# Kernel tuning notes

Hardware: AMD Instinct MI355X
Metric: run time of the kernel (lower is better)

Reference implementation:

```python
import jax, jax.numpy as jnp
import numpy as np

B, C, L = 64, 64, 8192
EPS = float(np.finfo(np.float32).eps)  # matches np.finfo(np.float32).eps in the torch code


def setup_inputs() -> dict:
    key = jax.random.key(0)
    k1, k2, k3 = jax.random.split(key, 3)
    data = jax.random.normal(k1, (B, C, L), dtype=jnp.float32)
    idxes = jax.random.randint(k2, (B, L), 0, L).astype(jnp.int32)
    # prefix lengths in [1, L] so every slice is non-empty (ragged branch)
    zero_pos = jax.random.randint(k3, (B,), 1, L + 1)
    return {"data": data, "idxes": idxes, "zero_pos": zero_pos}


def reference(data, idxes, zero_pos):
    # data: [B, C, L]; per-batch mean/std over the prefix data[b, :, :zero_pos[b]]
    Bn, Cn, Ln = data.shape
    mask = (jnp.arange(Ln)[None, :] < zero_pos[:, None])[:, None, :].astype(data.dtype)  # [B,1,L]
    cnt = Cn * zero_pos.astype(data.dtype)  # [B] number of elements in each prefix
    mean = jnp.sum(data * mask, axis=(1, 2)) / cnt  # [B]
    diff = (data - mean[:, None, None]) * mask  # [B,C,L]
    var = jnp.sum(diff * diff, axis=(1, 2)) / (cnt - 1.0)  # unbiased, as torch.std
    std = jnp.sqrt(var)  # [B]
    out = (data - mean[:, None, None]) / (std[:, None, None] + EPS)
    return (out, idxes, zero_pos)
```

## Files before the change

### kernel.cpp

```cpp
#include <hip/hip_runtime.h>
#include <hip/hip_bf16.h>
#include <math.h>

#define BB 64
#define CC 64
#define LL 8192
#define EPS_F 1.1920928955078125e-07f
#define SPLITS 32
#define NB_NORM 32768
#define NB_AUX  512


__global__ void tln_stats(const float* __restrict__ data,
                          const int* __restrict__ zero_pos,
                          float2* __restrict__ partials) {
    const int b = blockIdx.x;
    const int s = blockIdx.y;
    const int tid = threadIdx.x;
    const int zp = zero_pos[b];
    const int nv = zp >> 2;
    const float* base = data + (size_t)b * CC * LL;

    float sum = 0.0f, sq = 0.0f;
    for (int c = s; c < CC; c += SPLITS) {
        const float* rowp = base + (size_t)c * LL;
        const float4* row4 = (const float4*)rowp;
        for (int i = tid; i < nv; i += 256) {
            float4 v = row4[i];
            sum += v.x + v.y + v.z + v.w;
            sq  += v.x * v.x + v.y * v.y + v.z * v.z + v.w * v.w;
        }
        for (int l = (nv << 2) + tid; l < zp; l += 256) {
            float v = rowp[l];
            sum += v;
            sq  += v * v;
        }
    }

    #pragma unroll
    for (int off = 32; off > 0; off >>= 1) {
        sum += __shfl_down(sum, off);
        sq  += __shfl_down(sq, off);
    }
    __shared__ float lsum[4], lsq[4];
    const int wave = tid >> 6;
    const int lane = tid & 63;
    if (lane == 0) { lsum[wave] = sum; lsq[wave] = sq; }
    __syncthreads();
    if (tid == 0) {
        float2 p;
        p.x = lsum[0] + lsum[1] + lsum[2] + lsum[3];
        p.y = lsq[0] + lsq[1] + lsq[2] + lsq[3];
        partials[b * SPLITS + s] = p;
    }
}

__global__ void tln_fused(const float4* __restrict__ data4,
                          const float2* __restrict__ partials,
                          const int* __restrict__ zero_pos,
                          const int4* __restrict__ idxes,
                          float4* __restrict__ out4,
                          float4* __restrict__ out_idx,
                          float* __restrict__ out_zp) {
    const int blk = blockIdx.x;
    const int tid = threadIdx.x;

    if (blk < NB_NORM) {
        const int b = blk >> 9;
        __shared__ float s_m, s_inv;
        if (tid < 64) {
            float s_ = 0.0f, q_ = 0.0f;
            if (tid < SPLITS) {
                float2 p = partials[b * SPLITS + tid];
                s_ = p.x; q_ = p.y;
            }
            #pragma unroll
            for (int off = 16; off > 0; off >>= 1) {
                s_ += __shfl_down(s_, off);
                q_ += __shfl_down(q_, off);
            }
            if (tid == 0) {
                const float cnt = (float)CC * (float)zero_pos[b];
                const float mean = s_ / cnt;
                const float var = (q_ - cnt * mean * mean) / (cnt - 1.0f);
                s_m = mean;
                s_inv = 1.0f / (sqrtf(var) + EPS_F);
            }
        }
        __syncthreads();
        const float m = s_m, inv = s_inv;
        const size_t i = (size_t)blk * 256 + tid;
        float4 v = data4[i];
        float4 o;
        o.x = (v.x - m) * inv;
        o.y = (v.y - m) * inv;
        o.z = (v.z - m) * inv;
        o.w = (v.w - m) * inv;
        out4[i] = o;
    } else {
        const int j = blk - NB_NORM;
        const int i = j * 256 + tid;
        int4 v = idxes[i];
        float4 o;
        o.x = (float)v.x; o.y = (float)v.y; o.z = (float)v.z; o.w = (float)v.w;
        out_idx[i] = o;
        if (j == 0 && tid < BB) out_zp[tid] = (float)zero_pos[tid];
    }
}

extern "C" void kernel_launch(void* const* d_in, const int* in_sizes, int n_in,
                              void* d_out, int out_size, void* d_ws, size_t ws_size,
                              hipStream_t stream) {
    const float* data    = (const float*)d_in[0];
    const int* idxes     = (const int*)d_in[1];
    const int* zero_pos  = (const int*)d_in[2];

    float2* partials = (float2*)d_ws;

    float* out_data = (float*)d_out;
    float* out_idx  = out_data + (size_t)BB * CC * LL;
    float* out_zp   = out_idx + (size_t)BB * LL;

    tln_stats<<<dim3(BB, SPLITS), 256, 0, stream>>>(data, zero_pos, partials);

    tln_fused<<<NB_NORM + NB_AUX, 256, 0, stream>>>(
        (const float4*)data, partials, zero_pos, (const int4*)idxes,
        (float4*)out_data, (float4*)out_idx, out_zp);
}
```

Before: 249.6 us.

## Coarsen normalize blocks, drop LDS sync, use nontemporal stores

Each normalize block now processes eight float4 per thread (64 blocks per batch instead of 512), so the per-block stats reduction is amortised over more data. Every wave recomputes mean and inverse std with xor shuffles, which removes the shared-memory broadcast and the __syncthreads. Output and index stores use nontemporal hints so the write stream does not pollute the cache. Fewer blocks means less parallelism to hide latency, and the stats work is repeated in every wave.

```diff
diff --git a/kernel.cpp b/kernel.cpp
--- a/kernel.cpp
+++ b/kernel.cpp
@@ -1,5 +1,4 @@
 #include <hip/hip_runtime.h>
-#include <hip/hip_bf16.h>
 #include <math.h>
 
 #define BB 64
@@ -7,11 +6,16 @@
 #define LL 8192
 #define EPS_F 1.1920928955078125e-07f
 #define SPLITS 32
-#define NB_NORM 32768
+
+#define NORM_BLOCKS_PER_B 64
+#define NB_NORM (BB * NORM_BLOCKS_PER_B)
 #define NB_AUX  512
 
+typedef float f4 __attribute__((ext_vector_type(4)));
+typedef int   i4 __attribute__((ext_vector_type(4)));
 
-__global__ void tln_stats(const float* __restrict__ data,
+
+__global__ __launch_bounds__(256) void tln_stats(const float* __restrict__ data,
                           const int* __restrict__ zero_pos,
                           float2* __restrict__ partials) {
     const int b = blockIdx.x;
@@ -24,9 +28,9 @@
     float sum = 0.0f, sq = 0.0f;
     for (int c = s; c < CC; c += SPLITS) {
         const float* rowp = base + (size_t)c * LL;
-        const float4* row4 = (const float4*)rowp;
+        const f4* row4 = (const f4*)rowp;
         for (int i = tid; i < nv; i += 256) {
-            float4 v = row4[i];
+            f4 v = row4[i];
             sum += v.x + v.y + v.z + v.w;
             sq  += v.x * v.x + v.y * v.y + v.z * v.z + v.w * v.w;
         }
@@ -55,55 +59,47 @@
     }
 }
 
-__global__ void tln_fused(const float4* __restrict__ data4,
+__global__ __launch_bounds__(256) void tln_fused(const f4* __restrict__ data4,
                           const float2* __restrict__ partials,
                           const int* __restrict__ zero_pos,
-                          const int4* __restrict__ idxes,
-                          float4* __restrict__ out4,
-                          float4* __restrict__ out_idx,
+                          const i4* __restrict__ idxes,
+                          f4* __restrict__ out4,
+                          f4* __restrict__ out_idx,
                           float* __restrict__ out_zp) {
     const int blk = blockIdx.x;
     const int tid = threadIdx.x;
 
     if (blk < NB_NORM) {
-        const int b = blk >> 9;
-        __shared__ float s_m, s_inv;
-        if (tid < 64) {
-            float s_ = 0.0f, q_ = 0.0f;
-            if (tid < SPLITS) {
-                float2 p = partials[b * SPLITS + tid];
-                s_ = p.x; q_ = p.y;
-            }
-            #pragma unroll
-            for (int off = 16; off > 0; off >>= 1) {
-                s_ += __shfl_down(s_, off);
-                q_ += __shfl_down(q_, off);
-            }
-            if (tid == 0) {
-                const float cnt = (float)CC * (float)zero_pos[b];
-                const float mean = s_ / cnt;
-                const float var = (q_ - cnt * mean * mean) / (cnt - 1.0f);
-                s_m = mean;
-                s_inv = 1.0f / (sqrtf(var) + EPS_F);
-            }
+        const int b = blk >> 6;
+        const int t = blk & 63;
+        const int lane = tid & 63;
+
+        float2 p = partials[(b << 5) + (lane & 31)];
+        float s_ = p.x, q_ = p.y;
+        #pragma unroll
+        for (int off = 16; off > 0; off >>= 1) {
+            s_ += __shfl_xor(s_, off);
+            q_ += __shfl_xor(q_, off);
         }
-        __syncthreads();
-        const float m = s_m, inv = s_inv;
-        const size_t i = (size_t)blk * 256 + tid;
-        float4 v = data4[i];
-        float4 o;
-        o.x = (v.x - m) * inv;
-        o.y = (v.y - m) * inv;
-        o.z = (v.z - m) * inv;
-        o.w = (v.w - m) * inv;
-        out4[i] = o;
+        const float cnt  = (float)CC * (float)zero_pos[b];
+        const float mean = s_ / cnt;
+        const float var  = (q_ - cnt * mean * mean) / (cnt - 1.0f);
+        const float inv  = 1.0f / (sqrtf(var) + EPS_F);
+
+        const size_t base = ((size_t)b << 17) | ((size_t)t << 11) | (size_t)tid;
+        #pragma unroll
+        for (int k = 0; k < 8; ++k) {
+            const size_t i = base + ((size_t)k << 8);
+            f4 v = data4[i];
+            f4 o = (v - mean) * inv;
+            __builtin_nontemporal_store(o, out4 + i);
+        }
     } else {
         const int j = blk - NB_NORM;
         const int i = j * 256 + tid;
-        int4 v = idxes[i];
-        float4 o;
-        o.x = (float)v.x; o.y = (float)v.y; o.z = (float)v.z; o.w = (float)v.w;
-        out_idx[i] = o;
+        i4 v = idxes[i];
+        f4 o = __builtin_convertvector(v, f4);
+        __builtin_nontemporal_store(o, out_idx + i);
         if (j == 0 && tid < BB) out_zp[tid] = (float)zero_pos[tid];
     }
 }
@@ -124,6 +120,6 @@
     tln_stats<<<dim3(BB, SPLITS), 256, 0, stream>>>(data, zero_pos, partials);
 
     tln_fused<<<NB_NORM + NB_AUX, 256, 0, stream>>>(
-        (const float4*)data, partials, zero_pos, (const int4*)idxes,
-        (float4*)out_data, (float4*)out_idx, out_zp);
+        (const f4*)data, partials, zero_pos, (const i4*)idxes,
+        (f4*)out_data, (f4*)out_idx, out_zp);
 }
```

New measurement: 248.3 us. Within noise of the previous version (-0.5%).
